# Kernel optimization log

Measured on AMD Instinct MI355X. Metric: run time of the kernel, lower is better.

Reference implementation:

```python
import math
import jax, jax.numpy as jnp
import numpy as np

B, T, D, H, L = 8, 512, 128, 128, 2
W_SCALE = 0.05  # xavier-like small init to keep exp() input gate numerically sane


def setup_inputs() -> dict:
    key = jax.random.key(0)
    ks = jax.random.split(key, 14)
    inp = {"x": jax.random.normal(ks[0], (B, T, D), jnp.float32)}
    names_w = ["Wq", "Wk", "Wv", "Wi", "Wf", "Wo"]
    for j, nm in enumerate(names_w):
        inp[nm] = jax.random.normal(ks[1 + j], (L, H, D), jnp.float32) * W_SCALE
    # q/k/v biases zero-initialized per reset_parameters; gate biases random
    inp["bq"] = jnp.zeros((L, H), jnp.float32)
    inp["bk"] = jnp.zeros((L, H), jnp.float32)
    inp["bv"] = jnp.zeros((L, H), jnp.float32)
    inp["bi"] = jax.random.normal(ks[7], (L, H), jnp.float32) * W_SCALE
    inp["bf"] = jax.random.normal(ks[8], (L, H), jnp.float32) * W_SCALE
    inp["bo"] = jax.random.normal(ks[9], (L, H), jnp.float32) * W_SCALE
    return inp


def _mlstm_layer(xin, Wq, bq, Wk, bk, Wv, bv, Wi, bi, Wf, bf, Wo, bo):
    # xin: (B, T, Din). Precompute all 6 projections for the full sequence.
    q = jnp.einsum("btd,hd->bth", xin, Wq) + bq
    k = (jnp.einsum("btd,hd->bth", xin, Wk) + bk) * (1.0 / math.sqrt(H))
    v = jnp.einsum("btd,hd->bth", xin, Wv) + bv
    i = jnp.exp(jnp.einsum("btd,hd->bth", xin, Wi) + bi)
    f = jax.nn.sigmoid(jnp.einsum("btd,hd->bth", xin, Wf) + bf)
    o = jax.nn.sigmoid(jnp.einsum("btd,hd->bth", xin, Wo) + bo)

    def step(carry, qkvifo):
        C, n = carry                      # C: (B,H,H), n: (B,H)
        qt, kt, vt, it, ft, ot = qkvifo   # each (B,H)
        h_tilde = jnp.einsum("bij,bj->bi", C, qt)
        denom = jnp.maximum(jnp.abs(jnp.einsum("bi,bi->b", n, qt)), 1.0)[:, None]
        h = ot * (h_tilde / denom)
        n_new = ft * n + it * kt
        C_new = ft[:, :, None] * C + it[:, :, None] * (vt[:, :, None] * kt[:, None, :])
        return (C_new, n_new), h

    Bc = xin.shape[0]
    C0 = jnp.zeros((Bc, H, H), xin.dtype)
    n0 = jnp.zeros((Bc, H), xin.dtype)
    seq = tuple(jnp.swapaxes(a, 0, 1) for a in (q, k, v, i, f, o))  # (T,B,H)
    _, hs = jax.lax.scan(step, (C0, n0), seq)
    return jnp.swapaxes(hs, 0, 1)  # (B,T,H)


def reference(x, Wq, bq, Wk, bk, Wv, bv, Wi, bi, Wf, bf, Wo, bo):
    h = x
    for l in range(L):  # small fixed layer loop (dropout=0.0 -> identity)
        h = _mlstm_layer(h, Wq[l], bq[l], Wk[l], bk[l], Wv[l], bv[l],
                         Wi[l], bi[l], Wf[l], bf[l], Wo[l], bo[l])
    return h  # (B, T, H) output sequence of last layer
```

## Files before the change

### kernel.cpp

```cpp
#include <hip/hip_runtime.h>
#include <math.h>

#define BB 8
#define TT 512
#define DD 128
#define HH 128
#define BT_ (BB * TT)
#define CL 32
#define NCH 16
static const size_t BTH = (size_t)BT_ * HH;


struct WArgs { const float* W[6]; };
struct BArgs { const float* b[6]; };

template <int CTRL>
__device__ __forceinline__ float dpp_add(float x) {
  int y = __builtin_amdgcn_update_dpp(0, __builtin_bit_cast(int, x), CTRL,
                                      0xF, 0xF, true);
  return x + __builtin_bit_cast(float, y);
}

__global__ __launch_bounds__(256)
void transpose_w(WArgs w, float* __restrict__ Wt) {
  __shared__ float t[32][33];
  const int l = blockIdx.y / 6, p = blockIdx.y % 6;
  const float* src = w.W[p] + (size_t)l * HH * DD;
  float* dst = Wt + (size_t)blockIdx.y * HH * DD;
  const int ty0 = (blockIdx.x >> 2) * 32, tx0 = (blockIdx.x & 3) * 32;
  const int tx = threadIdx.x & 31, ty = threadIdx.x >> 5;
#pragma unroll
  for (int j = 0; j < 32; j += 8)
    t[ty + j][tx] = src[(size_t)(ty0 + ty + j) * DD + tx0 + tx];
  __syncthreads();
#pragma unroll
  for (int j = 0; j < 32; j += 8)
    dst[(size_t)(tx0 + ty + j) * HH + ty0 + tx] = t[tx][ty + j];
}

__global__ __launch_bounds__(256)
void proj_kernel(const float* __restrict__ X, const float* __restrict__ Wtl,
                 BArgs args, float* __restrict__ act) {
  __shared__ float xs[64][132];
  const int p = blockIdx.y;
  const int row0 = blockIdx.x * 64;
  const int tid = threadIdx.x;
  {
    const float4* xg = (const float4*)(X + (size_t)row0 * DD);
#pragma unroll
    for (int i = 0; i < 8; ++i) {
      int u = tid + 256 * i;
      float4 v = xg[u];
      *(float4*)&xs[u >> 5][(u & 31) * 4] = v;
    }
  }
  __syncthreads();

  const int h0 = (tid & 15) * 8;
  const int r0 = (tid >> 4) * 4;
  const float* wtp = Wtl + (size_t)p * HH * DD;

  float acc[4][8];
#pragma unroll
  for (int r = 0; r < 4; ++r)
#pragma unroll
    for (int j = 0; j < 8; ++j) acc[r][j] = 0.f;

  for (int d0 = 0; d0 < DD; d0 += 4) {
    float4 wa[4], wb[4];
#pragma unroll
    for (int i = 0; i < 4; ++i) {
      wa[i] = *(const float4*)(wtp + (size_t)(d0 + i) * HH + h0);
      wb[i] = *(const float4*)(wtp + (size_t)(d0 + i) * HH + h0 + 4);
    }
    float4 xr[4];
#pragma unroll
    for (int r = 0; r < 4; ++r) xr[r] = *(const float4*)&xs[r0 + r][d0];
#pragma unroll
    for (int i = 0; i < 4; ++i) {
#pragma unroll
      for (int r = 0; r < 4; ++r) {
        const float xv = (i == 0) ? xr[r].x
                        : (i == 1) ? xr[r].y
                        : (i == 2) ? xr[r].z : xr[r].w;
        acc[r][0] = fmaf(xv, wa[i].x, acc[r][0]);
        acc[r][1] = fmaf(xv, wa[i].y, acc[r][1]);
        acc[r][2] = fmaf(xv, wa[i].z, acc[r][2]);
        acc[r][3] = fmaf(xv, wa[i].w, acc[r][3]);
        acc[r][4] = fmaf(xv, wb[i].x, acc[r][4]);
        acc[r][5] = fmaf(xv, wb[i].y, acc[r][5]);
        acc[r][6] = fmaf(xv, wb[i].z, acc[r][6]);
        acc[r][7] = fmaf(xv, wb[i].w, acc[r][7]);
      }
    }
  }

  const float4 b0 = *(const float4*)(args.b[p] + h0);
  const float4 b1 = *(const float4*)(args.b[p] + h0 + 4);
  const float bias[8] = {b0.x, b0.y, b0.z, b0.w, b1.x, b1.y, b1.z, b1.w};
#pragma unroll
  for (int r = 0; r < 4; ++r) {
    const size_t row = (size_t)row0 + r0 + r;
    float v[8];
#pragma unroll
    for (int j = 0; j < 8; ++j) {
      float a = acc[r][j] + bias[j];
      if (p == 1)      a *= 0.088388347648318447f;
      else if (p == 3) a = __expf(a);
      else if (p >= 4) a = 1.0f / (1.0f + __expf(-a));
      v[j] = a;
    }
    if (p == 0) {
      float* dst = act + row * HH + h0;
      *(float4*)dst = make_float4(v[0], v[1], v[2], v[3]);
      *(float4*)(dst + 4) = make_float4(v[4], v[5], v[6], v[7]);
    } else if (p == 1) {
      float* dst = act + BTH + row * HH + h0;
      *(float4*)dst = make_float4(v[0], v[1], v[2], v[3]);
      *(float4*)(dst + 4) = make_float4(v[4], v[5], v[6], v[7]);
    } else if (p == 3 || p == 4) {
      float* dst = act + 2 * BTH + row * 2 * HH + 2 * h0 + (p == 3 ? 0 : 1);
#pragma unroll
      for (int j = 0; j < 8; ++j) dst[2 * j] = v[j];
    } else {
      float* dst = act + 4 * BTH + row * 2 * HH + 2 * h0 + (p == 2 ? 0 : 1);
#pragma unroll
      for (int j = 0; j < 8; ++j) dst[2 * j] = v[j];
    }
  }
}

__global__ __launch_bounds__(512)
void cseg2_kernel(const float* __restrict__ act, float* __restrict__ cbuf,
                  float* __restrict__ abuf, float* __restrict__ nbufB,
                  float* __restrict__ segA8, float* __restrict__ segB8) {
  __shared__ __align__(16) float kt[CL][128];
  __shared__ __align__(16) float ift[CL][64];
  __shared__ __align__(16) float vot[CL][64];
  const int tid = threadIdx.x;
  const int lane = tid & 63, wid = tid >> 6;
  const int blk = blockIdx.x;
  const int b = blk & 7, ch = (blk >> 3) & (NCH - 1), qtr = blk >> 7;
  const int t0 = ch * CL;
  const int p0 = qtr * 32;
  const size_t boff = (size_t)b * TT * HH;
  const float* kg = act + BTH + boff;
  const float* ifg = act + 2 * BTH + 2 * boff;
  const float* vog = act + 4 * BTH + 2 * boff;

#pragma unroll
  for (int i = 0; i < CL / 16; ++i) {
    const int u = tid + 512 * i;
    const int r = u >> 5, c = (u & 31) * 4;
    *(float4*)&kt[r][c] = *(const float4*)(kg + (size_t)(t0 + r) * HH + c);
  }
  {
    const int r = tid >> 4, c = (tid & 15) * 4;
    *(float4*)&ift[r][c] =
        *(const float4*)(ifg + (size_t)(t0 + r) * 2 * HH + 2 * p0 + c);
    *(float4*)&vot[r][c] =
        *(const float4*)(vog + (size_t)(t0 + r) * 2 * HH + 2 * p0 + c);
  }
  __syncthreads();

  const int pl = lane >> 4, cl = lane & 15;
  const int plocal = wid * 4 + pl;
  const int p = p0 + plocal;

  float C[8];
#pragma unroll
  for (int j = 0; j < 8; ++j) C[j] = 0.f;
  float Af = 1.f, Bn = 0.f, Aw = 1.f, Bw = 0.f;

#pragma unroll 4
  for (int t = 0; t < CL; ++t) {
    const float2 gif = *(const float2*)&ift[t][2 * plocal];
    const float2 gvo = *(const float2*)&vot[t][2 * plocal];
    const float4 k0 = *(const float4*)&kt[t][cl * 4];
    const float4 k1 = *(const float4*)&kt[t][cl * 4 + 64];
    const float kp = kt[t][p];
    const float a = gif.x * gvo.x;
    const float f = gif.y;
    C[0] = fmaf(f, C[0], a * k0.x);
    C[1] = fmaf(f, C[1], a * k0.y);
    C[2] = fmaf(f, C[2], a * k0.z);
    C[3] = fmaf(f, C[3], a * k0.w);
    C[4] = fmaf(f, C[4], a * k1.x);
    C[5] = fmaf(f, C[5], a * k1.y);
    C[6] = fmaf(f, C[6], a * k1.z);
    C[7] = fmaf(f, C[7], a * k1.w);
    Af *= f;
    Bn = fmaf(f, Bn, gif.x * kp);
    Aw *= f;
    Bw = fmaf(f, Bw, gif.x * kp);
    if ((t & 7) == 7) {
      if (cl == 0) {
        const size_t si = (size_t)(ch * 4 + (t >> 3)) * 1024 + b * 128 + p;
        segA8[si] = Aw;
        segB8[si] = Bw;
      }
      Aw = 1.f;
      Bw = 0.f;
    }
  }

  const size_t slot = (size_t)(b * 128 + p) * NCH + ch;
  *(float4*)(cbuf + slot * 128 + cl * 4) = make_float4(C[0], C[1], C[2], C[3]);
  *(float4*)(cbuf + slot * 128 + cl * 4 + 64) =
      make_float4(C[4], C[5], C[6], C[7]);
  if (cl == 0) {
    const size_t ci = (size_t)ch * 1024 + b * 128 + p;
    abuf[ci] = Af;
    nbufB[ci] = Bn;
  }
}

__global__ __launch_bounds__(512)
void hscan3_kernel(const float* __restrict__ act, float* __restrict__ hout,
                   const float* __restrict__ cbuf,
                   const float* __restrict__ abuf,
                   const float* __restrict__ nbufB,
                   const float* __restrict__ segA8,
                   const float* __restrict__ segB8) {
  __shared__ __align__(16) float qt[CL][128];
  __shared__ __align__(16) float kt[CL][128];
  __shared__ __align__(16) float iff[CL][256];
  __shared__ __align__(16) float vot[CL][64];
  __shared__ float den_part[4][8][2];
  __shared__ float den[CL];
  const int tid = threadIdx.x;
  const int lane = tid & 63, wid = tid >> 6;
  const int blk = blockIdx.x;
  const int b = blk & 7, ch = (blk >> 3) & (NCH - 1), qtr = blk >> 7;
  const int t0 = ch * CL;
  const int p0 = qtr * 32;
  const size_t boff = (size_t)b * TT * HH;
  const float* qg = act + boff;
  const float* kg = act + BTH + boff;
  const float* ifg = act + 2 * BTH + 2 * boff;
  const float* vog = act + 4 * BTH + 2 * boff;

#pragma unroll
  for (int i = 0; i < CL / 16; ++i) {
    const int u = tid + 512 * i;
    const int r = u >> 5, c = (u & 31) * 4;
    *(float4*)&qt[r][c] = *(const float4*)(qg + (size_t)(t0 + r) * HH + c);
    *(float4*)&kt[r][c] = *(const float4*)(kg + (size_t)(t0 + r) * HH + c);
  }
#pragma unroll
  for (int i = 0; i < 4; ++i) {
    const int u = tid + 512 * i;
    const int r = u >> 6, c = (u & 63) * 4;
    *(float4*)&iff[r][c] =
        *(const float4*)(ifg + (size_t)(t0 + r) * 2 * HH + c);
  }
  {
    const int r = tid >> 4, c = (tid & 15) * 4;
    *(float4*)&vot[r][c] =
        *(const float4*)(vog + (size_t)(t0 + r) * 2 * HH + 2 * p0 + c);
  }
  __syncthreads();

  {
    const int seg = tid >> 7, pd = tid & 127;
    const size_t cidx = (size_t)b * 128 + pd;
    float av[NCH], bv[NCH];
#pragma unroll
    for (int g = 0; g < NCH; ++g) {
      av[g] = abuf[(size_t)g * 1024 + cidx];
      bv[g] = nbufB[(size_t)g * 1024 + cidx];
    }
    float a8[3], b8[3];
#pragma unroll
    for (int s = 0; s < 3; ++s) {
      const size_t si = (size_t)(ch * 4 + s) * 1024 + cidx;
      a8[s] = segA8[si];
      b8[s] = segB8[si];
    }
    float n = 0.f;
#pragma unroll
    for (int g = 0; g < NCH; ++g)
      if (g < ch) n = fmaf(av[g], n, bv[g]);
#pragma unroll
    for (int s = 0; s < 3; ++s)
      if (s < seg) n = fmaf(a8[s], n, b8[s]);
    float prod[8];
#pragma unroll
    for (int j = 0; j < 8; ++j) {
      const int tl = seg * 8 + j;
      const float iv = iff[tl][2 * pd];
      const float fv = iff[tl][2 * pd + 1];
      prod[j] = n * qt[tl][pd];
      n = fmaf(fv, n, iv * kt[tl][pd]);
    }
#pragma unroll
    for (int j = 0; j < 8; ++j) {
      float s = prod[j];
      s = dpp_add<0x111>(s);
      s = dpp_add<0x112>(s);
      s = dpp_add<0x114>(s);
      s = dpp_add<0x118>(s);
      s = dpp_add<0x142>(s);
      s = dpp_add<0x143>(s);
      prod[j] = s;
    }
    if (lane == 63) {
#pragma unroll
      for (int j = 0; j < 8; ++j) den_part[seg][j][wid & 1] = prod[j];
    }
  }
  __syncthreads();
  if (tid < CL) {
    const int s_ = tid >> 3, j_ = tid & 7;
    const float d = den_part[s_][j_][0] + den_part[s_][j_][1];
    den[tid] = __builtin_amdgcn_rcpf(fmaxf(fabsf(d), 1.0f));
  }
  __syncthreads();
  {
    int u = tid;
    vot[u >> 5][2 * (u & 31) + 1] *= den[u >> 5];
    u = tid + 512;
    vot[u >> 5][2 * (u & 31) + 1] *= den[u >> 5];
  }
  __syncthreads();

  const int pl = lane >> 4, cl = lane & 15;
  const int plocal = wid * 4 + pl;
  const int p = p0 + plocal;

  float C[8];
#pragma unroll
  for (int j = 0; j < 8; ++j) C[j] = 0.f;
  {
    const size_t cb = (size_t)(b * 128 + p) * NCH;
#pragma unroll 1
    for (int g = 0; g < ch; ++g) {
      const float a = abuf[(size_t)g * 1024 + b * 128 + p];
      const float4 b0 = *(const float4*)(cbuf + (cb + g) * 128 + cl * 4);
      const float4 b1 = *(const float4*)(cbuf + (cb + g) * 128 + cl * 4 + 64);
      C[0] = fmaf(a, C[0], b0.x);
      C[1] = fmaf(a, C[1], b0.y);
      C[2] = fmaf(a, C[2], b0.z);
      C[3] = fmaf(a, C[3], b0.w);
      C[4] = fmaf(a, C[4], b1.x);
      C[5] = fmaf(a, C[5], b1.y);
      C[6] = fmaf(a, C[6], b1.z);
      C[7] = fmaf(a, C[7], b1.w);
    }
  }
  float* hbase = hout + boff + p;

#pragma unroll 4
  for (int t = 0; t < CL; ++t) {
    const float2 gif = *(const float2*)&iff[t][2 * p];
    const float2 gvo = *(const float2*)&vot[t][2 * plocal];
    const float4 q0 = *(const float4*)&qt[t][cl * 4];
    const float4 q1 = *(const float4*)&qt[t][cl * 4 + 64];
    const float4 k0 = *(const float4*)&kt[t][cl * 4];
    const float4 k1 = *(const float4*)&kt[t][cl * 4 + 64];
    float s0 = C[0] * q0.x;
    float s1 = C[4] * q1.x;
    s0 = fmaf(C[1], q0.y, s0);
    s1 = fmaf(C[5], q1.y, s1);
    s0 = fmaf(C[2], q0.z, s0);
    s1 = fmaf(C[6], q1.z, s1);
    s0 = fmaf(C[3], q0.w, s0);
    s1 = fmaf(C[7], q1.w, s1);
    float s = s0 + s1;
    const float a = gif.x * gvo.x;
    const float f = gif.y;
    C[0] = fmaf(f, C[0], a * k0.x);
    C[1] = fmaf(f, C[1], a * k0.y);
    C[2] = fmaf(f, C[2], a * k0.z);
    C[3] = fmaf(f, C[3], a * k0.w);
    C[4] = fmaf(f, C[4], a * k1.x);
    C[5] = fmaf(f, C[5], a * k1.y);
    C[6] = fmaf(f, C[6], a * k1.z);
    C[7] = fmaf(f, C[7], a * k1.w);
    s = dpp_add<0x111>(s);
    s = dpp_add<0x112>(s);
    s = dpp_add<0x114>(s);
    s = dpp_add<0x118>(s);
    if (cl == 15) hbase[(size_t)(t0 + t) * HH] = s * gvo.y;
  }
}

extern "C" void kernel_launch(void* const* d_in, const int* in_sizes, int n_in,
                              void* d_out, int out_size, void* d_ws,
                              size_t ws_size, hipStream_t stream) {
  (void)in_sizes; (void)n_in; (void)out_size; (void)ws_size;
  const float* x = (const float*)d_in[0];
  float* act = (float*)d_ws;
  float* hbuf = act + 6 * BTH;
  float* cbuf = act + 7 * BTH;
  float* abuf = cbuf + (size_t)1024 * NCH * 128;
  float* nbufB = abuf + 16384;
  float* segA8 = nbufB + 16384;
  float* segB8 = segA8 + 65536;
  float* Wt = (float*)d_out;

  WArgs wa;
  for (int j = 0; j < 6; ++j) wa.W[j] = (const float*)d_in[1 + j];
  transpose_w<<<dim3(16, 12), 256, 0, stream>>>(wa, Wt);

  for (int l = 0; l < 2; ++l) {
    BArgs ba;
    for (int j = 0; j < 6; ++j)
      ba.b[j] = (const float*)d_in[7 + j] + (size_t)l * HH;
    const float* wtl = Wt + (size_t)l * 6 * HH * DD;
    const float* xin = (l == 0) ? x : hbuf;
    float* hdst = (l == 0) ? hbuf : (float*)d_out;
    proj_kernel<<<dim3(BT_ / 64, 6), 256, 0, stream>>>(xin, wtl, ba, act);
    cseg2_kernel<<<512, 512, 0, stream>>>(act, cbuf, abuf, nbufB, segA8,
                                          segB8);
    hscan3_kernel<<<512, 512, 0, stream>>>(act, hdst, cbuf, abuf, nbufB,
                                           segA8, segB8);
  }
}
```

Measured before the change: 198.0 us.

## Add chunk-combine kernel so scan kernel reads precomputed start states

Adds a small kernel that runs the sequential prefix over chunk states for C, writing each chunk's starting state in place, and does a DPP-based parallel scan over the 8-step normalizer segments to produce per-segment starting n values. The scan kernel then loads one start state instead of re-folding all earlier chunks for C and n. This removes the redundant per-block serial prefix work, which grows with chunk index. The cost is one extra launch per layer and an extra round trip of the chunk-state buffer through global memory.

New measurement: 202.4 us. 1.02x slower.

```diff
diff --git a/kernel.cpp b/kernel.cpp
--- a/kernel.cpp
+++ b/kernel.cpp
@@ -19,6 +19,14 @@
   int y = __builtin_amdgcn_update_dpp(0, __builtin_bit_cast(int, x), CTRL,
                                       0xF, 0xF, true);
   return x + __builtin_bit_cast(float, y);
+}
+
+template <int CTRL>
+__device__ __forceinline__ float dpp_mov(float old, float x) {
+  int y = __builtin_amdgcn_update_dpp(__builtin_bit_cast(int, old),
+                                      __builtin_bit_cast(int, x), CTRL,
+                                      0xF, 0xF, false);
+  return __builtin_bit_cast(float, y);
 }
 
 __global__ __launch_bounds__(256)
@@ -132,8 +140,8 @@
 
 __global__ __launch_bounds__(512)
 void cseg2_kernel(const float* __restrict__ act, float* __restrict__ cbuf,
-                  float* __restrict__ abuf, float* __restrict__ nbufB,
-                  float* __restrict__ segA8, float* __restrict__ segB8) {
+                  float* __restrict__ abuf, float* __restrict__ segA8,
+                  float* __restrict__ segB8) {
   __shared__ __align__(16) float kt[CL][128];
   __shared__ __align__(16) float ift[CL][64];
   __shared__ __align__(16) float vot[CL][64];
@@ -170,7 +178,7 @@
   float C[8];
 #pragma unroll
   for (int j = 0; j < 8; ++j) C[j] = 0.f;
-  float Af = 1.f, Bn = 0.f, Aw = 1.f, Bw = 0.f;
+  float Af = 1.f, Aw = 1.f, Bw = 0.f;
 
 #pragma unroll 4
   for (int t = 0; t < CL; ++t) {
@@ -190,12 +198,11 @@
     C[6] = fmaf(f, C[6], a * k1.z);
     C[7] = fmaf(f, C[7], a * k1.w);
     Af *= f;
-    Bn = fmaf(f, Bn, gif.x * kp);
     Aw *= f;
     Bw = fmaf(f, Bw, gif.x * kp);
     if ((t & 7) == 7) {
       if (cl == 0) {
-        const size_t si = (size_t)(ch * 4 + (t >> 3)) * 1024 + b * 128 + p;
+        const size_t si = (size_t)(b * 128 + p) * 64 + ch * 4 + (t >> 3);
         segA8[si] = Aw;
         segB8[si] = Bw;
       }
@@ -208,20 +215,55 @@
   *(float4*)(cbuf + slot * 128 + cl * 4) = make_float4(C[0], C[1], C[2], C[3]);
   *(float4*)(cbuf + slot * 128 + cl * 4 + 64) =
       make_float4(C[4], C[5], C[6], C[7]);
-  if (cl == 0) {
-    const size_t ci = (size_t)ch * 1024 + b * 128 + p;
-    abuf[ci] = Af;
-    nbufB[ci] = Bn;
+  if (cl == 0) abuf[(size_t)ch * 1024 + b * 128 + p] = Af;
+}
+
+__global__ __launch_bounds__(128)
+void ccomb2_kernel(float* __restrict__ cbuf, const float* __restrict__ abuf,
+                   const float* __restrict__ segA8,
+                   const float* __restrict__ segB8,
+                   float* __restrict__ nstart) {
+  const int chain = blockIdx.x;
+  const int c = threadIdx.x;
+  float A[NCH], Bv[NCH];
+#pragma unroll
+  for (int g = 0; g < NCH; ++g) {
+    A[g] = abuf[(size_t)g * 1024 + chain];
+    Bv[g] = cbuf[((size_t)chain * NCH + g) * 128 + c];
+  }
+  float Cs = 0.f;
+#pragma unroll
+  for (int g = 0; g < NCH; ++g) {
+    cbuf[((size_t)chain * NCH + g) * 128 + c] = Cs;
+    Cs = fmaf(A[g], Cs, Bv[g]);
+  }
+  if (c < 64) {
+    const int lane = c;
+    float a = segA8[(size_t)chain * 64 + lane];
+    float bn = segB8[(size_t)chain * 64 + lane];
+#define SCAN_LVL(CTRL)                          \
+  {                                             \
+    float As = dpp_mov<CTRL>(1.0f, a);          \
+    float Bs = dpp_mov<CTRL>(0.0f, bn);         \
+    bn = fmaf(a, Bs, bn);                       \
+    a = a * As;                                 \
+  }
+    SCAN_LVL(0x111)
+    SCAN_LVL(0x112)
+    SCAN_LVL(0x114)
+    SCAN_LVL(0x118)
+    SCAN_LVL(0x142)
+    SCAN_LVL(0x143)
+#undef SCAN_LVL
+    const int idx = (lane + 1) & 63;
+    nstart[(size_t)idx * 1024 + chain] = (lane == 63) ? 0.f : bn;
   }
 }
 
 __global__ __launch_bounds__(512)
 void hscan3_kernel(const float* __restrict__ act, float* __restrict__ hout,
                    const float* __restrict__ cbuf,
-                   const float* __restrict__ abuf,
-                   const float* __restrict__ nbufB,
-                   const float* __restrict__ segA8,
-                   const float* __restrict__ segB8) {
+                   const float* __restrict__ nstart) {
   __shared__ __align__(16) float qt[CL][128];
   __shared__ __align__(16) float kt[CL][128];
   __shared__ __align__(16) float iff[CL][256];
@@ -263,27 +305,7 @@
 
   {
     const int seg = tid >> 7, pd = tid & 127;
-    const size_t cidx = (size_t)b * 128 + pd;
-    float av[NCH], bv[NCH];
-#pragma unroll
-    for (int g = 0; g < NCH; ++g) {
-      av[g] = abuf[(size_t)g * 1024 + cidx];
-      bv[g] = nbufB[(size_t)g * 1024 + cidx];
-    }
-    float a8[3], b8[3];
-#pragma unroll
-    for (int s = 0; s < 3; ++s) {
-      const size_t si = (size_t)(ch * 4 + s) * 1024 + cidx;
-      a8[s] = segA8[si];
-      b8[s] = segB8[si];
-    }
-    float n = 0.f;
-#pragma unroll
-    for (int g = 0; g < NCH; ++g)
-      if (g < ch) n = fmaf(av[g], n, bv[g]);
-#pragma unroll
-    for (int s = 0; s < 3; ++s)
-      if (s < seg) n = fmaf(a8[s], n, b8[s]);
+    float n = nstart[(size_t)(ch * 4 + seg) * 1024 + b * 128 + pd];
     float prod[8];
 #pragma unroll
     for (int j = 0; j < 8; ++j) {
@@ -329,24 +351,12 @@
   const int p = p0 + plocal;
 
   float C[8];
-#pragma unroll
-  for (int j = 0; j < 8; ++j) C[j] = 0.f;
-  {
-    const size_t cb = (size_t)(b * 128 + p) * NCH;
-#pragma unroll 1
-    for (int g = 0; g < ch; ++g) {
-      const float a = abuf[(size_t)g * 1024 + b * 128 + p];
-      const float4 b0 = *(const float4*)(cbuf + (cb + g) * 128 + cl * 4);
-      const float4 b1 = *(const float4*)(cbuf + (cb + g) * 128 + cl * 4 + 64);
-      C[0] = fmaf(a, C[0], b0.x);
-      C[1] = fmaf(a, C[1], b0.y);
-      C[2] = fmaf(a, C[2], b0.z);
-      C[3] = fmaf(a, C[3], b0.w);
-      C[4] = fmaf(a, C[4], b1.x);
-      C[5] = fmaf(a, C[5], b1.y);
-      C[6] = fmaf(a, C[6], b1.z);
-      C[7] = fmaf(a, C[7], b1.w);
-    }
+  {
+    const size_t slot = ((size_t)(b * 128 + p) * NCH + ch) * 128;
+    const float4 c0 = *(const float4*)(cbuf + slot + cl * 4);
+    const float4 c1 = *(const float4*)(cbuf + slot + cl * 4 + 64);
+    C[0] = c0.x; C[1] = c0.y; C[2] = c0.z; C[3] = c0.w;
+    C[4] = c1.x; C[5] = c1.y; C[6] = c1.z; C[7] = c1.w;
   }
   float* hbase = hout + boff + p;
 
@@ -394,9 +404,9 @@
   float* hbuf = act + 6 * BTH;
   float* cbuf = act + 7 * BTH;
   float* abuf = cbuf + (size_t)1024 * NCH * 128;
-  float* nbufB = abuf + 16384;
-  float* segA8 = nbufB + 16384;
+  float* segA8 = abuf + 16384;
   float* segB8 = segA8 + 65536;
+  float* nstart = segB8 + 65536;
   float* Wt = (float*)d_out;
 
   WArgs wa;
@@ -411,9 +421,8 @@
     const float* xin = (l == 0) ? x : hbuf;
     float* hdst = (l == 0) ? hbuf : (float*)d_out;
     proj_kernel<<<dim3(BT_ / 64, 6), 256, 0, stream>>>(xin, wtl, ba, act);
-    cseg2_kernel<<<512, 512, 0, stream>>>(act, cbuf, abuf, nbufB, segA8,
-                                          segB8);
-    hscan3_kernel<<<512, 512, 0, stream>>>(act, hdst, cbuf, abuf, nbufB,
-                                           segA8, segB8);
-  }
-}
+    cseg2_kernel<<<512, 512, 0, stream>>>(act, cbuf, abuf, segA8, segB8);
+    ccomb2_kernel<<<1024, 128, 0, stream>>>(cbuf, abuf, segA8, segB8, nstart);
+    hscan3_kernel<<<512, 512, 0, stream>>>(act, hdst, cbuf, nstart);
+  }
+}
```
